# Performance work log

Hardware: AMD Instinct MI355X
Metric: run time of the kernel (lower is better)

## Reference

```python
import jax, jax.numpy as jnp
import numpy as np

K = 4
TEMPERATURE = 30.0


def setup_inputs() -> dict:
    key = jax.random.key(0)
    ks = jax.random.split(key, 6)
    B, C, H, W_sp = 32, 128, 56, 56
    Cout, kh, kw = 128, 3, 3
    Cred = max(C // 4, 1)
    x = jax.random.normal(ks[0], (B, C, H, W_sp), dtype=jnp.float32)
    # K parallel conv kernels + biases (fan-in scaled init)
    fan = C * kh * kw
    W = jax.random.normal(ks[1], (K, Cout, C, kh, kw), dtype=jnp.float32) / np.sqrt(fan)
    b = jax.random.normal(ks[2], (K, Cout), dtype=jnp.float32) * 0.01
    # attention branch: 1x1 convs == dense on pooled features
    aw1 = jax.random.normal(ks[3], (Cred, C), dtype=jnp.float32) / np.sqrt(C)
    aw2 = jax.random.normal(ks[4], (K, Cred), dtype=jnp.float32) / np.sqrt(Cred)
    return {"x": x, "W": W, "b": b, "aw1": aw1, "aw2": aw2}


def reference(x, W, b, aw1, aw2):
    # attention: global avg pool -> 1x1 conv (dense) -> relu -> 1x1 conv -> softmax(logits/T)
    pooled = jnp.mean(x, axis=(2, 3))                       # [B, C]
    h1 = jax.nn.relu(jnp.einsum('bc,rc->br', pooled, aw1))  # [B, Cred]
    logits = jnp.einsum('br,kr->bk', h1, aw2)               # [B, K]
    attn = jax.nn.softmax(logits / TEMPERATURE, axis=1)     # [B, K]

    pad = 1
    out = None
    for i in range(K):  # fixed small K, structurally distinct kernels
        yi = jax.lax.conv_general_dilated(
            x, W[i], window_strides=(1, 1), padding=[(pad, pad), (pad, pad)],
            dimension_numbers=('NCHW', 'OIHW', 'NCHW'))
        yi = yi + b[i][None, :, None, None]
        yi = yi * attn[:, i][:, None, None, None]
        out = yi if out is None else out + yi
    return out
```

## Files before the change

kernel.cpp:

```cpp
#include <hip/hip_runtime.h>
#include <hip/hip_bf16.h>
#include <stdint.h>

typedef __bf16 bf16x8 __attribute__((ext_vector_type(8)));
typedef float  f32x4  __attribute__((ext_vector_type(4)));
typedef unsigned short u16x8 __attribute__((ext_vector_type(8)));

#define NB 32
#define NC 128
#define NH 56
#define NW 56
#define NK 4
#define NCO 128
#define NCR 32
#define NHW 3136
#define TEMPER 30.0f

#define WS_ATTN   0u
#define WS_BC     4096u
#define WS_ROWSUM 65536u
#define WS_WC     1048576u
#define WS_XT     10485760u

__global__ void xt_kernel(const float* __restrict__ x, __hip_bfloat16* __restrict__ xt,
                          float* __restrict__ rowsum) {
  __shared__ float lds[58 * 133];
  int xcd = blockIdx.x & 7;
  int j   = blockIdx.x >> 3;
  int b   = xcd * 4 + j / 58;
  int hp  = j % 58;
  int blk = b * 58 + hp;
  int h = hp - 1;
  bool hin = (h >= 0) && (h < NH);
  int tid = threadIdx.x;
  if (hin) {
    const float* xrow = x + ((size_t)b * NC) * NHW + (size_t)h * NW;
    for (int i = tid; i < 128 * 14; i += 256) {
      int c = i / 14;
      int w4 = (i - c * 14) * 4;
      float4 v = *(const float4*)(xrow + (size_t)c * NHW + w4);
      int base = (w4 + 1) * 133 + c;
      lds[base]         = v.x;
      lds[base + 133]   = v.y;
      lds[base + 2*133] = v.z;
      lds[base + 3*133] = v.w;
    }
  }
  __syncthreads();
  __hip_bfloat16* orow = xt + (size_t)blk * (58 * 128);
  for (int i = tid; i < 58 * 16; i += 256) {
    int wp = i >> 4;
    int cg = (i & 15) << 3;
    u16x8 o;
    if (!hin || wp == 0 || wp == 57) {
      o = (u16x8)0;
    } else {
      const float* src = lds + wp * 133 + cg;
      #pragma unroll
      for (int jx = 0; jx < 8; ++jx) {
        union { __hip_bfloat16 b; unsigned short u; } cv;
        cv.b = __float2bfloat16(src[jx]);
        o[jx] = cv.u;
      }
    }
    *(u16x8*)(orow + wp * 128 + cg) = o;
  }
  if (hin && tid < 128) {
    float s = 0.f;
    #pragma unroll 8
    for (int wp = 1; wp <= 56; ++wp) s += lds[wp * 133 + tid];
    rowsum[(size_t)blk * 128 + tid] = s;
  }
}

__global__ void attn_kernel(const float* __restrict__ rowsum, const float* __restrict__ aw1,
                            const float* __restrict__ aw2, const float* __restrict__ bias,
                            float* __restrict__ attn, float* __restrict__ bc_out) {
  int b = blockIdx.x;
  __shared__ float sp[NC], h1[NCR], at[NK];
  int t = threadIdx.x;
  if (t < NC) {
    float s = 0.f;
    for (int hp = 1; hp <= 56; ++hp) s += rowsum[((size_t)b * 58 + hp) * 128 + t];
    sp[t] = s * (1.0f / (float)NHW);
  }
  __syncthreads();
  if (t < NCR) {
    float s = 0.f;
    for (int c = 0; c < NC; ++c) s += aw1[t*NC + c] * sp[c];
    h1[t] = s > 0.f ? s : 0.f;
  }
  __syncthreads();
  if (t == 0) {
    float lg[NK], mx = -1e30f;
    for (int k = 0; k < NK; ++k) {
      float s = 0.f;
      for (int r = 0; r < NCR; ++r) s += aw2[k*NCR + r] * h1[r];
      lg[k] = s * (1.0f/TEMPER);
      mx = fmaxf(mx, lg[k]);
    }
    float den = 0.f, e[NK];
    for (int k = 0; k < NK; ++k) { e[k] = expf(lg[k]-mx); den += e[k]; }
    float inv = 1.0f/den;
    for (int k = 0; k < NK; ++k) { at[k] = e[k]*inv; attn[b*NK+k] = at[k]; }
  }
  __syncthreads();
  if (t < NCO) {
    float s = 0.f;
    for (int k = 0; k < NK; ++k) s += at[k] * bias[k*NCO + t];
    bc_out[b*NCO + t] = s;
  }
}

__global__ void combine_kernel(const float* __restrict__ W, const float* __restrict__ attn,
                               __hip_bfloat16* __restrict__ wc) {
  int gid = blockIdx.x;
  int bg  = gid >> 6;
  int tcell = (gid & 63) * 256 + threadIdx.x;
  int co = tcell >> 7, ci = tcell & 127;
  float w[4][9];
  const float* wp = W + ((size_t)co * 128 + ci) * 9;
  #pragma unroll
  for (int k = 0; k < 4; ++k)
    #pragma unroll
    for (int j = 0; j < 9; ++j)
      w[k][j] = wp[(size_t)k * 147456 + j];
  for (int b = bg * 8; b < bg * 8 + 8; ++b) {
    float a0 = attn[b*4+0], a1 = attn[b*4+1], a2 = attn[b*4+2], a3 = attn[b*4+3];
    #pragma unroll
    for (int j = 0; j < 9; ++j) {
      float v = a0*w[0][j] + a1*w[1][j] + a2*w[2][j] + a3*w[3][j];
      wc[(((size_t)b*9 + j) * 128 + co) * 128 + ci] = __float2bfloat16(v);
    }
  }
}

#define RS 2368
#define CS 40

#define GLOAD16(src, dst) \
  __builtin_amdgcn_global_load_lds( \
    (const __attribute__((address_space(1))) unsigned int*)(src), \
    (__attribute__((address_space(3))) unsigned int*)(dst), 16, 0, 0)

#define SB() __builtin_amdgcn_sched_barrier(0)

__global__ __launch_bounds__(256, 2) void conv_kernel(
    const unsigned short* __restrict__ xt,
    const unsigned short* __restrict__ wc,
    const float* __restrict__ bc,
    float* __restrict__ out) {
  __shared__ __align__(16) unsigned short lds_b[1792*8];
  __shared__ __align__(16) unsigned short lds_a[3*4096];
  const int tid  = threadIdx.x;
  const int lane = tid & 63;
  const int wv   = tid >> 6;
  const int wm   = wv & 1;
  const int wn   = wv >> 1;
  const int bid  = blockIdx.x;
  const int xcd  = bid & 7;
  const int jj   = bid >> 3;
  const int b    = xcd*4 + jj/14;
  const int r0   = (jj % 14) * 4;
  const int li   = lane & 15;
  const int kg   = lane >> 4;

  int srcB[7];
  #pragma unroll
  for (int i = 0; i < 7; ++i) {
    int q = i*256 + tid;
    int r = q / 296;
    int sl = q - r*296;
    int col = sl / 5;
    int part = sl - col*5;
    int rc = r > 5 ? 5 : r;
    int cl = col > 57 ? 57 : col;
    int pc = part > 3 ? 3 : part;
    srcB[i] = ((r0 + rc)*58 + cl)*128 + pc*8;
  }
  int srcA[6];
  #pragma unroll
  for (int i = 0; i < 6; ++i) {
    int c = i*256 + tid;
    int kwl  = c >> 9;
    int co   = (c & 511) >> 2;
    int part = c & 3;
    srcA[i] = (kwl*128 + co)*128 + part*8;
  }

  int xoff[7];
  #pragma unroll
  for (int f = 0; f < 7; ++f) {
    int pos = wn*112 + f*16 + li;
    int rB = pos / 56;
    int cB = pos - rB*56;
    xoff[f] = rB*RS + cB*CS + kg*8;
  }
  const int aRead = (wm*64 + li)*32 + kg*8;

  const f32x4 vzero = {0.f, 0.f, 0.f, 0.f};
  f32x4 acc[4][7];
  #pragma unroll
  for (int mo = 0; mo < 4; ++mo)
    #pragma unroll
    for (int f = 0; f < 7; ++f) acc[mo][f] = vzero;

  const unsigned short* xtg = xt + (size_t)b*(58*58*128);
  const unsigned short* wcg = wc + (size_t)b*(9*128*128);

  #define LOADFRAG(AF, BF, kwl, kh) do { \
    _Pragma("unroll") \
    for (int mo = 0; mo < 4; ++mo) \
      AF[mo] = *(const bf16x8*)(lds_a + (kwl)*4096 + aRead + mo*512); \
    _Pragma("unroll") \
    for (int f = 0; f < 7; ++f) \
      BF[f] = *(const bf16x8*)(lds_b + xoff[f] + (kh)*RS + (kwl)*CS); \
  } while (0)

  #define DOMFMA(AF, BF) do { \
    __builtin_amdgcn_s_setprio(1); \
    _Pragma("unroll") \
    for (int mo = 0; mo < 4; ++mo) \
      _Pragma("unroll") \
      for (int f = 0; f < 7; ++f) \
        acc[mo][f] = __builtin_amdgcn_mfma_f32_16x16x32_bf16(AF[mo], BF[f], acc[mo][f], 0, 0, 0); \
    __builtin_amdgcn_s_setprio(0); \
  } while (0)

  for (int cc = 0; cc < 4; ++cc) {
    #pragma unroll
    for (int kh = 0; kh < 3; ++kh) {
      __syncthreads();
      #pragma unroll
      for (int i = 0; i < 6; ++i)
        GLOAD16(wcg + kh*49152 + srcA[i] + cc*32, lds_a + (i*256 + wv*64)*8);
      if (kh == 0) {
        #pragma unroll
        for (int i = 0; i < 7; ++i)
          GLOAD16(xtg + srcB[i] + cc*32, lds_b + (i*256 + wv*64)*8);
      }
      __syncthreads();

      bf16x8 afE[4], bfE[7], afO[4], bfO[7];
      LOADFRAG(afE, bfE, 0, kh);
      SB();
      LOADFRAG(afO, bfO, 1, kh);
      SB();
      DOMFMA(afE, bfE);
      SB();
      LOADFRAG(afE, bfE, 2, kh);
      SB();
      DOMFMA(afO, bfO);
      SB();
      DOMFMA(afE, bfE);
    }
  }

  float* ob = out + (size_t)b*NCO*NHW;
  #pragma unroll
  for (int mo = 0; mo < 4; ++mo) {
    #pragma unroll
    for (int rg = 0; rg < 4; ++rg) {
      const int co = wm*64 + mo*16 + kg*4 + rg;
      const float bv = bc[b*NCO + co];
      float* orow = ob + (size_t)co*NHW;
      #pragma unroll
      for (int f = 0; f < 7; ++f) {
        int pos = wn*112 + f*16 + li;
        int rB = pos / 56;
        int cB = pos - rB*56;
        orow[(r0 + rB)*56 + cB] = acc[mo][f][rg] + bv;
      }
    }
  }
}

extern "C" void kernel_launch(void* const* d_in, const int* in_sizes, int n_in,
                              void* d_out, int out_size, void* d_ws, size_t ws_size,
                              hipStream_t stream) {
  const float* x   = (const float*)d_in[0];
  const float* W   = (const float*)d_in[1];
  const float* bia = (const float*)d_in[2];
  const float* aw1 = (const float*)d_in[3];
  const float* aw2 = (const float*)d_in[4];
  float* out = (float*)d_out;
  char* ws = (char*)d_ws;
  float* attn   = (float*)(ws + WS_ATTN);
  float* bcm    = (float*)(ws + WS_BC);
  float* rowsum = (float*)(ws + WS_ROWSUM);
  __hip_bfloat16* wc = (__hip_bfloat16*)(ws + WS_WC);
  __hip_bfloat16* xt = (__hip_bfloat16*)(ws + WS_XT);

  xt_kernel<<<NB*58, 256, 0, stream>>>(x, xt, rowsum);
  attn_kernel<<<NB, 128, 0, stream>>>(rowsum, aw1, aw2, bia, attn, bcm);
  combine_kernel<<<256, 256, 0, stream>>>(W, attn, wc);
  conv_kernel<<<448, 256, 0, stream>>>((const unsigned short*)xt,
                                       (const unsigned short*)wc, bcm, out);
}
```

Measured before the change: 66.35 us.

## Load conv weight fragments directly from global into registers, dropping weight LDS staging

The weight (A) operand is no longer staged through shared memory. Each wave now reads its bf16 weight fragments straight from global memory into registers, double-buffered one kernel tap ahead of the MFMAs. This removes the per-kh weight LDS stores, the reads back out of LDS and two barriers per kh step, leaving only one pair of barriers per channel chunk for the input tile. The cost is more global/L2 traffic, since the two waves sharing wm read the same weights, and global-load latency now sits directly in front of each MFMA group.

Result: slower. 74.87 us (+12.8%).

```diff
diff --git a/kernel.cpp b/kernel.cpp
--- a/kernel.cpp
+++ b/kernel.cpp
@@ -151,7 +151,6 @@
     const float* __restrict__ bc,
     float* __restrict__ out) {
   __shared__ __align__(16) unsigned short lds_b[1792*8];
-  __shared__ __align__(16) unsigned short lds_a[3*4096];
   const int tid  = threadIdx.x;
   const int lane = tid & 63;
   const int wv   = tid >> 6;
@@ -178,15 +177,6 @@
     int pc = part > 3 ? 3 : part;
     srcB[i] = ((r0 + rc)*58 + cl)*128 + pc*8;
   }
-  int srcA[6];
-  #pragma unroll
-  for (int i = 0; i < 6; ++i) {
-    int c = i*256 + tid;
-    int kwl  = c >> 9;
-    int co   = (c & 511) >> 2;
-    int part = c & 3;
-    srcA[i] = (kwl*128 + co)*128 + part*8;
-  }
 
   int xoff[7];
   #pragma unroll
@@ -196,7 +186,6 @@
     int cB = pos - rB*56;
     xoff[f] = rB*RS + cB*CS + kg*8;
   }
-  const int aRead = (wm*64 + li)*32 + kg*8;
 
   const f32x4 vzero = {0.f, 0.f, 0.f, 0.f};
   f32x4 acc[4][7];
@@ -206,54 +195,52 @@
     for (int f = 0; f < 7; ++f) acc[mo][f] = vzero;
 
   const unsigned short* xtg = xt + (size_t)b*(58*58*128);
-  const unsigned short* wcg = wc + (size_t)b*(9*128*128);
-
-  #define LOADFRAG(AF, BF, kwl, kh) do { \
+  const unsigned short* wcA = wc + (size_t)b*(9*128*128) + (wm*64 + li)*128 + kg*8;
+
+  #define LOADA(DST, khw, cc) do { \
     _Pragma("unroll") \
     for (int mo = 0; mo < 4; ++mo) \
-      AF[mo] = *(const bf16x8*)(lds_a + (kwl)*4096 + aRead + mo*512); \
+      DST[mo] = *(const bf16x8*)(wcA + (khw)*16384 + mo*2048 + (cc)*32); \
+  } while (0)
+
+  #define GROUP(g, CUR, NXT, cc) do { \
+    if ((g) < 8) { LOADA(NXT, (g)+1, cc); SB(); } \
+    const int kh_ = (g)/3, kw_ = (g)-kh_*3; \
+    const int koff_ = kh_*RS + kw_*CS; \
+    bf16x8 bfr[7]; \
     _Pragma("unroll") \
     for (int f = 0; f < 7; ++f) \
-      BF[f] = *(const bf16x8*)(lds_b + xoff[f] + (kh)*RS + (kwl)*CS); \
-  } while (0)
-
-  #define DOMFMA(AF, BF) do { \
+      bfr[f] = *(const bf16x8*)(lds_b + xoff[f] + koff_); \
+    SB(); \
     __builtin_amdgcn_s_setprio(1); \
     _Pragma("unroll") \
     for (int mo = 0; mo < 4; ++mo) \
       _Pragma("unroll") \
       for (int f = 0; f < 7; ++f) \
-        acc[mo][f] = __builtin_amdgcn_mfma_f32_16x16x32_bf16(AF[mo], BF[f], acc[mo][f], 0, 0, 0); \
+        acc[mo][f] = __builtin_amdgcn_mfma_f32_16x16x32_bf16(CUR[mo], bfr[f], acc[mo][f], 0, 0, 0); \
     __builtin_amdgcn_s_setprio(0); \
+    SB(); \
   } while (0)
 
   for (int cc = 0; cc < 4; ++cc) {
-    #pragma unroll
-    for (int kh = 0; kh < 3; ++kh) {
-      __syncthreads();
-      #pragma unroll
-      for (int i = 0; i < 6; ++i)
-        GLOAD16(wcg + kh*49152 + srcA[i] + cc*32, lds_a + (i*256 + wv*64)*8);
-      if (kh == 0) {
-        #pragma unroll
-        for (int i = 0; i < 7; ++i)
-          GLOAD16(xtg + srcB[i] + cc*32, lds_b + (i*256 + wv*64)*8);
-      }
-      __syncthreads();
-
-      bf16x8 afE[4], bfE[7], afO[4], bfO[7];
-      LOADFRAG(afE, bfE, 0, kh);
-      SB();
-      LOADFRAG(afO, bfO, 1, kh);
-      SB();
-      DOMFMA(afE, bfE);
-      SB();
-      LOADFRAG(afE, bfE, 2, kh);
-      SB();
-      DOMFMA(afO, bfO);
-      SB();
-      DOMFMA(afE, bfE);
-    }
+    bf16x8 afE[4], afO[4];
+    LOADA(afE, 0, cc);
+    SB();
+    __syncthreads();
+    #pragma unroll
+    for (int i = 0; i < 7; ++i)
+      GLOAD16(xtg + srcB[i] + cc*32, lds_b + (i*256 + wv*64)*8);
+    __syncthreads();
+
+    GROUP(0, afE, afO, cc);
+    GROUP(1, afO, afE, cc);
+    GROUP(2, afE, afO, cc);
+    GROUP(3, afO, afE, cc);
+    GROUP(4, afE, afO, cc);
+    GROUP(5, afO, afE, cc);
+    GROUP(6, afE, afO, cc);
+    GROUP(7, afO, afE, cc);
+    GROUP(8, afE, afO, cc);
   }
 
   float* ob = out + (size_t)b*NCO*NHW;
```
